# Kernel tuning notes

Measured on AMD Instinct MI355X. Metric: run time of the kernel, lower is better.

The kernel has to match this reference:

```python
import jax, jax.numpy as jnp
import numpy as np

N, E = 100000, 1600000
D_IN, D_HID, D_OUT = 128, 128, 64


def setup_inputs() -> dict:
    key = jax.random.key(0)
    ks = jax.random.split(key, 12)
    x = jax.random.normal(ks[0], (N, D_IN), dtype=jnp.float32)
    edge_index = jax.random.randint(ks[1], (2, E), 0, N, dtype=jnp.int32)

    def glorot(k, fan_in, fan_out):
        lim = np.sqrt(6.0 / (fan_in + fan_out)).astype(np.float32)
        return jax.random.uniform(k, (fan_in, fan_out), jnp.float32, -lim, lim)

    return {
        "x": x,
        "edge_index": edge_index,
        "W_l0": glorot(ks[2], D_IN, D_HID), "W_r0": glorot(ks[3], D_IN, D_HID), "b0": jnp.zeros((D_HID,), jnp.float32),
        "W_l1": glorot(ks[4], D_HID, D_HID), "W_r1": glorot(ks[5], D_HID, D_HID), "b1": jnp.zeros((D_HID,), jnp.float32),
        "W_l2": glorot(ks[6], D_HID, D_OUT), "W_r2": glorot(ks[7], D_HID, D_OUT), "b2": jnp.zeros((D_OUT,), jnp.float32),
    }


def _sage_conv(x, src, dst, W_l, W_r, b):
    # mean aggregation of source features onto destination nodes
    msg = jnp.take(x, src, axis=0)                               # [E, d]
    agg = jax.ops.segment_sum(msg, dst, num_segments=N)          # [N, d]
    deg = jax.ops.segment_sum(jnp.ones_like(dst, x.dtype), dst, num_segments=N)
    agg = agg / jnp.maximum(deg, 1.0)[:, None]
    # out = lin_l(aggr) + lin_r(x); lin_l has bias (PyG SAGEConv convention)
    return agg @ W_l + x @ W_r + b


def reference(x, edge_index, W_l0, W_r0, b0, W_l1, W_r1, b1, W_l2, W_r2, b2):
    src, dst = edge_index[0], edge_index[1]
    h = jax.nn.relu(_sage_conv(x, src, dst, W_l0, W_r0, b0))
    h = jax.nn.relu(_sage_conv(h, src, dst, W_l1, W_r1, b1))
    # dropout is identity in eval mode
    return _sage_conv(h, src, dst, W_l2, W_r2, b2)
```

## Files before the change

### kernel.cpp

```cpp
#include <hip/hip_runtime.h>
#include <hip/hip_bf16.h>
#include <stdint.h>

#define D 128
#define BSH 8
#define BKN 256
#define TILE 4096
#define CAPB 5376

typedef __attribute__((ext_vector_type(8))) short short8;
typedef __attribute__((ext_vector_type(4))) float f32x4;

typedef __attribute__((address_space(1))) const void gvoid;
typedef __attribute__((address_space(3))) void lvoid;

__device__ inline float bf16lo(uint32_t u){ return __uint_as_float(u << 16); }
__device__ inline float bf16hi(uint32_t u){ return __uint_as_float(u & 0xffff0000u); }
__device__ inline unsigned short f2bf(float f){
    union { __hip_bfloat16 h; unsigned short u; } cvt;
    cvt.h = __float2bfloat16(f);
    return cvt.u;
}

#define ACC8(q) \
    acc[0] += bf16lo(q.x); acc[1] += bf16hi(q.x); \
    acc[2] += bf16lo(q.y); acc[3] += bf16hi(q.y); \
    acc[4] += bf16lo(q.z); acc[5] += bf16hi(q.z); \
    acc[6] += bf16lo(q.w); acc[7] += bf16hi(q.w);

__global__ __launch_bounds__(256) void prep_and_bin(
    const int* __restrict__ src, const int* __restrict__ dst,
    int* __restrict__ bfill, uint32_t* __restrict__ binbuf, int E, int nbk, int nBin,
    const float* __restrict__ Wl0, const float* __restrict__ Wr0,
    const float* __restrict__ Wl1, const float* __restrict__ Wr1,
    const float* __restrict__ Wl2, const float* __restrict__ Wr2,
    unsigned short* __restrict__ WT0, unsigned short* __restrict__ WT1,
    unsigned short* __restrict__ WT2)
{
    __shared__ int hist[400];
    __shared__ int cur[400];
    int t = threadIdx.x;
    if ((int)blockIdx.x < nBin){
        int tile0 = blockIdx.x * TILE;
        int cnt = min(TILE, E - tile0);
        for (int i = t; i < nbk; i += 256) hist[i] = 0;
        __syncthreads();
        for (int i = t; i < cnt; i += 256)
            atomicAdd(&hist[dst[tile0 + i] >> BSH], 1);
        __syncthreads();
        for (int i = t; i < nbk; i += 256){
            int h = hist[i];
            int base = h ? atomicAdd(&bfill[i], h) : 0;
            cur[i] = i * CAPB + base;
        }
        __syncthreads();
        for (int i = t; i < cnt; i += 256){
            int d = dst[tile0 + i];
            int b = d >> BSH;
            int p = atomicAdd(&cur[b], 1);
            binbuf[p] = (uint32_t)src[tile0 + i] | ((uint32_t)(d & (BKN - 1)) << 17);
        }
    } else {
        int idx = ((int)blockIdx.x - nBin) * 256 + t;
        if (idx < 32768){
            int k = idx & 127, j = idx >> 7;
            WT0[j * 128 + k] = f2bf(j < 128 ? Wl0[k * 128 + j] : Wr0[k * 128 + (j - 128)]);
        } else if (idx < 65536){
            int i = idx - 32768; int k = i & 127, j = i >> 7;
            WT1[j * 128 + k] = f2bf(j < 128 ? Wl1[k * 128 + j] : Wr1[k * 128 + (j - 128)]);
        } else if (idx < 81920){
            int i = idx - 65536; int k = i & 127, j = i >> 7;
            WT2[j * 128 + k] = f2bf(j < 64 ? Wl2[k * 64 + j] : Wr2[k * 64 + (j - 64)]);
        }
    }
}

__global__ __launch_bounds__(256, 3) void gemm0_fill(
    const float* __restrict__ xf, const unsigned short* __restrict__ WT,
    const float* __restrict__ bias, unsigned short* __restrict__ ylz, int n,
    const uint32_t* __restrict__ binbuf, const int* __restrict__ bcnt,
    int* __restrict__ roff, int* __restrict__ rend, int* __restrict__ csr,
    int nbk, int gG)
{
    __shared__ __align__(16) char smem[128 * 256];
    int tid = threadIdx.x;

    if ((int)blockIdx.x < nbk){
        int* hist  = (int*)smem;
        int* hist2 = hist + 256;
        int* hb    = hist2 + 256;
        int* sc    = hb + 256;
        int b = blockIdx.x, t = tid;
        int e0 = b * CAPB;
        int e1 = e0 + bcnt[b];
        int v0 = b << BSH;
        int nv = min(BKN, n - v0);

        hist[t] = 0; hist2[t] = 0;
        __syncthreads();
        for (int e = e0 + t; e < e1; e += 256)
            atomicAdd(&hist[binbuf[e] >> 17], 1);
        __syncthreads();
        int own = hist[t];
        sc[t] = own;
        __syncthreads();
        for (int o = 1; o < 256; o <<= 1){
            int x = (t >= o) ? sc[t - o] : 0;
            __syncthreads();
            sc[t] += x;
            __syncthreads();
        }
        int ex = sc[t] - own;
        hb[t] = ex;
        if (t < nv){
            roff[v0 + t] = e0 + ex;
            rend[v0 + t] = e0 + ex + own;
        }
        __syncthreads();
        for (int e = e0 + t; e < e1; e += 256){
            uint32_t p = binbuf[e];
            int local = p >> 17;
            int pos = e0 + hb[local] + atomicAdd(&hist2[local], 1);
            csr[pos] = (int)(p & 0x1FFFFu);
        }
        return;
    }

    int bid = (int)blockIdx.x - nbk;
    int bx = bid % gG, by = bid / gG;
    char* As = smem;
    int lane = tid & 63, wave = tid >> 6;
    int rbase = bx * 128;
    int lrow = lane & 15, lk = (lane >> 4) * 8;
    int colbase = by * 128 + wave * 32;

    short8 bfr[4][2];
    #pragma unroll
    for (int kk = 0; kk < 4; kk++)
        #pragma unroll
        for (int cf = 0; cf < 2; cf++)
            bfr[kk][cf] = *reinterpret_cast<const short8*>(
                WT + (size_t)(colbase + cf * 16 + lrow) * 128 + kk * 32 + lk);

    {
        int cb = (tid & 15) * 16;
        #pragma unroll
        for (int i = 0; i < 8; i++){
            int row = i * 16 + (tid >> 4);
            int grow = min(rbase + row, n - 1);
            const float* p = xf + (size_t)grow * 128 + (cb >> 1);
            float4 f0 = *reinterpret_cast<const float4*>(p);
            float4 f1 = *reinterpret_cast<const float4*>(p + 4);
            uint4 q;
            q.x = (uint32_t)f2bf(f0.x) | ((uint32_t)f2bf(f0.y) << 16);
            q.y = (uint32_t)f2bf(f0.z) | ((uint32_t)f2bf(f0.w) << 16);
            q.z = (uint32_t)f2bf(f1.x) | ((uint32_t)f2bf(f1.y) << 16);
            q.w = (uint32_t)f2bf(f1.z) | ((uint32_t)f2bf(f1.w) << 16);
            *reinterpret_cast<uint4*>(As + row * 256 + (cb ^ ((row & 7) << 4))) = q;
        }
    }
    __syncthreads();

    f32x4 acc[8][2];
    #pragma unroll
    for (int fr = 0; fr < 8; fr++)
        #pragma unroll
        for (int cf = 0; cf < 2; cf++)
            acc[fr][cf] = (f32x4){0.f, 0.f, 0.f, 0.f};

    #pragma unroll
    for (int kk = 0; kk < 4; kk++){
        int cb = kk * 64 + (lane >> 4) * 16;
        #pragma unroll
        for (int fr = 0; fr < 8; fr++){
            int row = fr * 16 + lrow;
            short8 a = *reinterpret_cast<const short8*>(As + row * 256 + (cb ^ ((row & 7) << 4)));
            #pragma unroll
            for (int cf = 0; cf < 2; cf++)
                acc[fr][cf] = __builtin_amdgcn_mfma_f32_16x16x32_bf16(bfr[kk][cf], a, acc[fr][cf], 0, 0, 0);
        }
    }

    float4 bv[2];
    #pragma unroll
    for (int cf = 0; cf < 2; cf++){
        int cg = colbase + cf * 16 + (lane >> 4) * 4;
        bv[cf] = (cg >= 128) ? *reinterpret_cast<const float4*>(bias + (cg - 128))
                             : (float4){0.f, 0.f, 0.f, 0.f};
    }

    #pragma unroll
    for (int fr = 0; fr < 8; fr++){
        int row = rbase + fr * 16 + lrow;
        if (row < n){
            #pragma unroll
            for (int cf = 0; cf < 2; cf++){
                int cg = colbase + cf * 16 + (lane >> 4) * 4;
                uint2 o;
                o.x = (uint32_t)f2bf(acc[fr][cf][0] + bv[cf].x) |
                      ((uint32_t)f2bf(acc[fr][cf][1] + bv[cf].y) << 16);
                o.y = (uint32_t)f2bf(acc[fr][cf][2] + bv[cf].z) |
                      ((uint32_t)f2bf(acc[fr][cf][3] + bv[cf].w) << 16);
                *reinterpret_cast<uint2*>(ylz + (size_t)row * 256 + cg) = o;
            }
        }
    }
}

template<int NC>
__global__ __launch_bounds__(256, 3) void dense_gemm(
    const unsigned short* __restrict__ xb,
    const unsigned short* __restrict__ WT, const float* __restrict__ bias,
    unsigned short* __restrict__ ylz, int n)
{
    constexpr int DOUT = NC / 2;
    __shared__ __align__(16) char As[128 * 256];
    int tid = threadIdx.x, lane = tid & 63, wave = tid >> 6;
    int rbase = blockIdx.x * 128;
    int lrow = lane & 15, lk = (lane >> 4) * 8;
    int colbase = blockIdx.y * 128 + wave * 32;

    short8 bfr[4][2];
    #pragma unroll
    for (int kk = 0; kk < 4; kk++)
        #pragma unroll
        for (int cf = 0; cf < 2; cf++)
            bfr[kk][cf] = *reinterpret_cast<const short8*>(
                WT + (size_t)(colbase + cf * 16 + lrow) * 128 + kk * 32 + lk);

    {
        int cb = (lane & 15) * 16;
        #pragma unroll
        for (int i = 0; i < 8; i++){
            int row = i * 16 + (tid >> 4);
            int grow = min(rbase + row, n - 1);
            const unsigned short* gsrc = xb + (size_t)grow * 128 + ((cb ^ ((row & 7) << 4)) >> 1);
            __builtin_amdgcn_global_load_lds(
                (gvoid*)gsrc,
                (lvoid*)(As + (i * 16 + wave * 4) * 256),
                16, 0, 0);
        }
    }
    __syncthreads();

    f32x4 acc[8][2];
    #pragma unroll
    for (int fr = 0; fr < 8; fr++)
        #pragma unroll
        for (int cf = 0; cf < 2; cf++)
            acc[fr][cf] = (f32x4){0.f, 0.f, 0.f, 0.f};

    #pragma unroll
    for (int kk = 0; kk < 4; kk++){
        int cb = kk * 64 + (lane >> 4) * 16;
        #pragma unroll
        for (int fr = 0; fr < 8; fr++){
            int row = fr * 16 + lrow;
            short8 a = *reinterpret_cast<const short8*>(As + row * 256 + (cb ^ ((row & 7) << 4)));
            #pragma unroll
            for (int cf = 0; cf < 2; cf++)
                acc[fr][cf] = __builtin_amdgcn_mfma_f32_16x16x32_bf16(bfr[kk][cf], a, acc[fr][cf], 0, 0, 0);
        }
    }

    float4 bv[2];
    #pragma unroll
    for (int cf = 0; cf < 2; cf++){
        int cg = colbase + cf * 16 + (lane >> 4) * 4;
        bv[cf] = (cg >= DOUT) ? *reinterpret_cast<const float4*>(bias + (cg - DOUT))
                              : (float4){0.f, 0.f, 0.f, 0.f};
    }

    #pragma unroll
    for (int fr = 0; fr < 8; fr++){
        int row = rbase + fr * 16 + lrow;
        if (row < n){
            #pragma unroll
            for (int cf = 0; cf < 2; cf++){
                int cg = colbase + cf * 16 + (lane >> 4) * 4;
                uint2 o;
                o.x = (uint32_t)f2bf(acc[fr][cf][0] + bv[cf].x) |
                      ((uint32_t)f2bf(acc[fr][cf][1] + bv[cf].y) << 16);
                o.y = (uint32_t)f2bf(acc[fr][cf][2] + bv[cf].z) |
                      ((uint32_t)f2bf(acc[fr][cf][3] + bv[cf].w) << 16);
                *reinterpret_cast<uint2*>(ylz + (size_t)row * NC + cg) = o;
            }
        }
    }
}

__global__ __launch_bounds__(256, 4) void agg_relu(
    const unsigned short* __restrict__ ylz, const int* __restrict__ roff,
    const int* __restrict__ rend,
    const int* __restrict__ csr, unsigned short* __restrict__ hout, int n)
{
    int grp = threadIdx.x >> 4, li = threadIdx.x & 15;
    int v = blockIdx.x * 16 + grp;
    if (v >= n) return;
    int s0 = roff[v], s1 = rend[v];
    const unsigned short* base = ylz + li * 8;
    float acc[8] = {0.f,0.f,0.f,0.f,0.f,0.f,0.f,0.f};
    int e = s0;
    for (; e + 8 <= s1; e += 8){
        int i0=csr[e],i1=csr[e+1],i2=csr[e+2],i3=csr[e+3];
        int i4=csr[e+4],i5=csr[e+5],i6=csr[e+6],i7=csr[e+7];
        uint4 q0 = *reinterpret_cast<const uint4*>(base + (size_t)i0 * 256);
        uint4 q1 = *reinterpret_cast<const uint4*>(base + (size_t)i1 * 256);
        uint4 q2 = *reinterpret_cast<const uint4*>(base + (size_t)i2 * 256);
        uint4 q3 = *reinterpret_cast<const uint4*>(base + (size_t)i3 * 256);
        uint4 q4 = *reinterpret_cast<const uint4*>(base + (size_t)i4 * 256);
        uint4 q5 = *reinterpret_cast<const uint4*>(base + (size_t)i5 * 256);
        uint4 q6 = *reinterpret_cast<const uint4*>(base + (size_t)i6 * 256);
        uint4 q7 = *reinterpret_cast<const uint4*>(base + (size_t)i7 * 256);
        ACC8(q0) ACC8(q1) ACC8(q2) ACC8(q3) ACC8(q4) ACC8(q5) ACC8(q6) ACC8(q7)
    }
    if (e < s1){
        int last = s1 - 1;
        int i0=csr[e];
        int i1=csr[min(e+1,last)],i2=csr[min(e+2,last)],i3=csr[min(e+3,last)];
        int i4=csr[min(e+4,last)],i5=csr[min(e+5,last)],i6=csr[min(e+6,last)],i7=csr[min(e+7,last)];
        uint4 z4 = make_uint4(0,0,0,0);
        uint4 q0 = *reinterpret_cast<const uint4*>(base + (size_t)i0 * 256);
        uint4 q1 = *reinterpret_cast<const uint4*>(base + (size_t)i1 * 256);
        uint4 q2 = *reinterpret_cast<const uint4*>(base + (size_t)i2 * 256);
        uint4 q3 = *reinterpret_cast<const uint4*>(base + (size_t)i3 * 256);
        uint4 q4 = *reinterpret_cast<const uint4*>(base + (size_t)i4 * 256);
        uint4 q5 = *reinterpret_cast<const uint4*>(base + (size_t)i5 * 256);
        uint4 q6 = *reinterpret_cast<const uint4*>(base + (size_t)i6 * 256);
        uint4 q7 = *reinterpret_cast<const uint4*>(base + (size_t)i7 * 256);
        if (e+1 > last) q1 = z4;
        if (e+2 > last) q2 = z4;
        if (e+3 > last) q3 = z4;
        if (e+4 > last) q4 = z4;
        if (e+5 > last) q5 = z4;
        if (e+6 > last) q6 = z4;
        if (e+7 > last) q7 = z4;
        ACC8(q0) ACC8(q1) ACC8(q2) ACC8(q3) ACC8(q4) ACC8(q5) ACC8(q6) ACC8(q7)
    }
    int d = s1 - s0;
    float inv = (d > 0) ? 1.0f / (float)d : 0.0f;
    uint4 zq = *reinterpret_cast<const uint4*>(ylz + (size_t)v * 256 + 128 + li * 8);
    float z0=bf16lo(zq.x), z1=bf16hi(zq.x), z2=bf16lo(zq.y), z3=bf16hi(zq.y);
    float z4_=bf16lo(zq.z), z5=bf16hi(zq.z), z6=bf16lo(zq.w), z7=bf16hi(zq.w);
    uint4 o;
    o.x = (uint32_t)f2bf(fmaxf(acc[0]*inv+z0,0.f)) | ((uint32_t)f2bf(fmaxf(acc[1]*inv+z1,0.f)) << 16);
    o.y = (uint32_t)f2bf(fmaxf(acc[2]*inv+z2,0.f)) | ((uint32_t)f2bf(fmaxf(acc[3]*inv+z3,0.f)) << 16);
    o.z = (uint32_t)f2bf(fmaxf(acc[4]*inv+z4_,0.f)) | ((uint32_t)f2bf(fmaxf(acc[5]*inv+z5,0.f)) << 16);
    o.w = (uint32_t)f2bf(fmaxf(acc[6]*inv+z6,0.f)) | ((uint32_t)f2bf(fmaxf(acc[7]*inv+z7,0.f)) << 16);
    *reinterpret_cast<uint4*>(hout + (size_t)v * 128 + li * 8) = o;
}

__global__ __launch_bounds__(256, 4) void agg_out64(
    const unsigned short* __restrict__ ylz, const int* __restrict__ roff,
    const int* __restrict__ rend,
    const int* __restrict__ csr, float* __restrict__ out, int n)
{
    int grp = threadIdx.x >> 3, li = threadIdx.x & 7;
    int v = blockIdx.x * 32 + grp;
    if (v >= n) return;
    int s0 = roff[v], s1 = rend[v];
    const unsigned short* base = ylz + li * 8;
    float acc[8] = {0.f,0.f,0.f,0.f,0.f,0.f,0.f,0.f};
    int e = s0;
    for (; e + 8 <= s1; e += 8){
        int i0=csr[e],i1=csr[e+1],i2=csr[e+2],i3=csr[e+3];
        int i4=csr[e+4],i5=csr[e+5],i6=csr[e+6],i7=csr[e+7];
        uint4 q0 = *reinterpret_cast<const uint4*>(base + (size_t)i0 * 128);
        uint4 q1 = *reinterpret_cast<const uint4*>(base + (size_t)i1 * 128);
        uint4 q2 = *reinterpret_cast<const uint4*>(base + (size_t)i2 * 128);
        uint4 q3 = *reinterpret_cast<const uint4*>(base + (size_t)i3 * 128);
        uint4 q4 = *reinterpret_cast<const uint4*>(base + (size_t)i4 * 128);
        uint4 q5 = *reinterpret_cast<const uint4*>(base + (size_t)i5 * 128);
        uint4 q6 = *reinterpret_cast<const uint4*>(base + (size_t)i6 * 128);
        uint4 q7 = *reinterpret_cast<const uint4*>(base + (size_t)i7 * 128);
        ACC8(q0) ACC8(q1) ACC8(q2) ACC8(q3) ACC8(q4) ACC8(q5) ACC8(q6) ACC8(q7)
    }
    if (e < s1){
        int last = s1 - 1;
        int i0=csr[e];
        int i1=csr[min(e+1,last)],i2=csr[min(e+2,last)],i3=csr[min(e+3,last)];
        int i4=csr[min(e+4,last)],i5=csr[min(e+5,last)],i6=csr[min(e+6,last)],i7=csr[min(e+7,last)];
        uint4 z4 = make_uint4(0,0,0,0);
        uint4 q0 = *reinterpret_cast<const uint4*>(base + (size_t)i0 * 128);
        uint4 q1 = *reinterpret_cast<const uint4*>(base + (size_t)i1 * 128);
        uint4 q2 = *reinterpret_cast<const uint4*>(base + (size_t)i2 * 128);
        uint4 q3 = *reinterpret_cast<const uint4*>(base + (size_t)i3 * 128);
        uint4 q4 = *reinterpret_cast<const uint4*>(base + (size_t)i4 * 128);
        uint4 q5 = *reinterpret_cast<const uint4*>(base + (size_t)i5 * 128);
        uint4 q6 = *reinterpret_cast<const uint4*>(base + (size_t)i6 * 128);
        uint4 q7 = *reinterpret_cast<const uint4*>(base + (size_t)i7 * 128);
        if (e+1 > last) q1 = z4;
        if (e+2 > last) q2 = z4;
        if (e+3 > last) q3 = z4;
        if (e+4 > last) q4 = z4;
        if (e+5 > last) q5 = z4;
        if (e+6 > last) q6 = z4;
        if (e+7 > last) q7 = z4;
        ACC8(q0) ACC8(q1) ACC8(q2) ACC8(q3) ACC8(q4) ACC8(q5) ACC8(q6) ACC8(q7)
    }
    int d = s1 - s0;
    float inv = (d > 0) ? 1.0f / (float)d : 0.0f;
    uint4 zq = *reinterpret_cast<const uint4*>(ylz + (size_t)v * 128 + 64 + li * 8);
    float4 o0, o1;
    o0.x = acc[0]*inv + bf16lo(zq.x);
    o0.y = acc[1]*inv + bf16hi(zq.x);
    o0.z = acc[2]*inv + bf16lo(zq.y);
    o0.w = acc[3]*inv + bf16hi(zq.y);
    o1.x = acc[4]*inv + bf16lo(zq.z);
    o1.y = acc[5]*inv + bf16hi(zq.z);
    o1.z = acc[6]*inv + bf16lo(zq.w);
    o1.w = acc[7]*inv + bf16hi(zq.w);
    *reinterpret_cast<float4*>(out + (size_t)v * 64 + li * 8) = o0;
    *reinterpret_cast<float4*>(out + (size_t)v * 64 + li * 8 + 4) = o1;
}

extern "C" void kernel_launch(void* const* d_in, const int* in_sizes, int n_in,
                              void* d_out, int out_size, void* d_ws, size_t ws_size,
                              hipStream_t stream)
{
    const float* x   = (const float*)d_in[0];
    const int*   ei  = (const int*)d_in[1];
    const float* Wl0 = (const float*)d_in[2];
    const float* Wr0 = (const float*)d_in[3];
    const float* b0  = (const float*)d_in[4];
    const float* Wl1 = (const float*)d_in[5];
    const float* Wr1 = (const float*)d_in[6];
    const float* b1  = (const float*)d_in[7];
    const float* Wl2 = (const float*)d_in[8];
    const float* Wr2 = (const float*)d_in[9];
    const float* b2  = (const float*)d_in[10];

    int N = in_sizes[0] / D;
    int E = in_sizes[1] / 2;
    const int* src = ei;
    const int* dst = ei + E;
    int NBK = (N + BKN - 1) >> BSH;

    char* ws = (char*)d_ws;
    size_t off = 0;
    auto alloc = [&](size_t bytes) -> void* {
        void* p = ws + off;
        off = (off + bytes + 255) & ~(size_t)255;
        return p;
    };
    int*      bfill  = (int*)alloc((size_t)NBK * 4);
    int*      roff   = (int*)alloc((size_t)N * 4);
    int*      rend   = (int*)alloc((size_t)N * 4);
    int*      csr    = (int*)alloc((size_t)NBK * CAPB * 4);
    unsigned short* ylz = (unsigned short*)alloc((size_t)N * 256 * 2);
    unsigned short* h0  = (unsigned short*)alloc((size_t)N * D * 2);
    unsigned short* h1  = (unsigned short*)alloc((size_t)N * D * 2);
    unsigned short* WT0 = (unsigned short*)alloc((size_t)256 * 128 * 2);
    unsigned short* WT1 = (unsigned short*)alloc((size_t)256 * 128 * 2);
    unsigned short* WT2 = (unsigned short*)alloc((size_t)128 * 128 * 2);
    uint32_t* binbuf = (uint32_t*)alloc((size_t)NBK * CAPB * 4);

    hipMemsetAsync(bfill, 0, (size_t)NBK * 4, stream);

    int nBin = (E + TILE - 1) / TILE;
    int gG = (N + 127) / 128;
    int gA = (N + 15) / 16;
    int gA2 = (N + 31) / 32;

    prep_and_bin<<<nBin + 320, 256, 0, stream>>>(
        src, dst, bfill, binbuf, E, NBK, nBin,
        Wl0, Wr0, Wl1, Wr1, Wl2, Wr2, WT0, WT1, WT2);

    gemm0_fill<<<NBK + gG * 2, 256, 0, stream>>>(
        x, WT0, b0, ylz, N, binbuf, bfill, roff, rend, csr, NBK, gG);

    agg_relu<<<gA, 256, 0, stream>>>(ylz, roff, rend, csr, h0, N);
    dense_gemm<256><<<dim3(gG, 2), 256, 0, stream>>>(h0, WT1, b1, ylz, N);
    agg_relu<<<gA, 256, 0, stream>>>(ylz, roff, rend, csr, h1, N);
    dense_gemm<128><<<dim3(gG, 1), 256, 0, stream>>>(h1, WT2, b2, ylz, N);
    agg_out64<<<gA2, 256, 0, stream>>>(ylz, roff, rend, csr, (float*)d_out, N);
}
```

Baseline: 262.9 us.

## Store aggregated features in column-sliced layout so gathers hit compact per-slice arrays

The GEMM outputs that get gathered are now split into 8 feature slices of 16 (or 8) bf16 columns each, stored slice-major. Each aggregation block handles one slice for many nodes, so the working set of a gather pass is a small array that may stay in L2/MALL rather than striding across full rows. The root (z) half is written to a separate contiguous buffer. Buffers are aliased (binbuf onto h1sl, layer-2 outputs onto h0sl) to reduce the workspace footprint. In exchange, each edge index is now read 8 times, once per slice, and the GEMM input loads use a strided sliced addressing.

```diff
diff --git a/kernel.cpp b/kernel.cpp
--- a/kernel.cpp
+++ b/kernel.cpp
@@ -77,7 +77,8 @@
 
 __global__ __launch_bounds__(256, 3) void gemm0_fill(
     const float* __restrict__ xf, const unsigned short* __restrict__ WT,
-    const float* __restrict__ bias, unsigned short* __restrict__ ylz, int n,
+    const float* __restrict__ bias, unsigned short* __restrict__ ysl,
+    unsigned short* __restrict__ z, int n,
     const uint32_t* __restrict__ binbuf, const int* __restrict__ bcnt,
     int* __restrict__ roff, int* __restrict__ rend, int* __restrict__ csr,
     int nbk, int gG)
@@ -133,6 +134,7 @@
     int rbase = bx * 128;
     int lrow = lane & 15, lk = (lane >> 4) * 8;
     int colbase = by * 128 + wave * 32;
+    size_t n16 = (size_t)n * 16;
 
     short8 bfr[4][2];
     #pragma unroll
@@ -201,7 +203,10 @@
                       ((uint32_t)f2bf(acc[fr][cf][1] + bv[cf].y) << 16);
                 o.y = (uint32_t)f2bf(acc[fr][cf][2] + bv[cf].z) |
                       ((uint32_t)f2bf(acc[fr][cf][3] + bv[cf].w) << 16);
-                *reinterpret_cast<uint2*>(ylz + (size_t)row * 256 + cg) = o;
+                if (cg < 128)
+                    *reinterpret_cast<uint2*>(ysl + (size_t)(cg >> 4) * n16 + (size_t)row * 16 + (cg & 15)) = o;
+                else
+                    *reinterpret_cast<uint2*>(z + (size_t)row * 128 + (cg - 128)) = o;
             }
         }
     }
@@ -211,14 +216,17 @@
 __global__ __launch_bounds__(256, 3) void dense_gemm(
     const unsigned short* __restrict__ xb,
     const unsigned short* __restrict__ WT, const float* __restrict__ bias,
-    unsigned short* __restrict__ ylz, int n)
+    unsigned short* __restrict__ ysl, unsigned short* __restrict__ z, int n)
 {
     constexpr int DOUT = NC / 2;
+    constexpr int SL = DOUT / 8;
     __shared__ __align__(16) char As[128 * 256];
     int tid = threadIdx.x, lane = tid & 63, wave = tid >> 6;
     int rbase = blockIdx.x * 128;
     int lrow = lane & 15, lk = (lane >> 4) * 8;
     int colbase = blockIdx.y * 128 + wave * 32;
+    size_t n16 = (size_t)n * 16;
+    size_t nSL = (size_t)n * SL;
 
     short8 bfr[4][2];
     #pragma unroll
@@ -234,7 +242,9 @@
         for (int i = 0; i < 8; i++){
             int row = i * 16 + (tid >> 4);
             int grow = min(rbase + row, n - 1);
-            const unsigned short* gsrc = xb + (size_t)grow * 128 + ((cb ^ ((row & 7) << 4)) >> 1);
+            int cbx = cb ^ ((row & 7) << 4);
+            const unsigned short* gsrc = xb + (size_t)(cbx >> 5) * n16
+                                            + (size_t)grow * 16 + ((cbx & 31) >> 1);
             __builtin_amdgcn_global_load_lds(
                 (gvoid*)gsrc,
                 (lvoid*)(As + (i * 16 + wave * 4) * 256),
@@ -283,35 +293,39 @@
                       ((uint32_t)f2bf(acc[fr][cf][1] + bv[cf].y) << 16);
                 o.y = (uint32_t)f2bf(acc[fr][cf][2] + bv[cf].z) |
                       ((uint32_t)f2bf(acc[fr][cf][3] + bv[cf].w) << 16);
-                *reinterpret_cast<uint2*>(ylz + (size_t)row * NC + cg) = o;
+                if (cg < DOUT)
+                    *reinterpret_cast<uint2*>(ysl + (size_t)(cg / SL) * nSL + (size_t)row * SL + (cg % SL)) = o;
+                else
+                    *reinterpret_cast<uint2*>(z + (size_t)row * DOUT + (cg - DOUT)) = o;
             }
         }
     }
 }
 
-__global__ __launch_bounds__(256, 4) void agg_relu(
-    const unsigned short* __restrict__ ylz, const int* __restrict__ roff,
-    const int* __restrict__ rend,
-    const int* __restrict__ csr, unsigned short* __restrict__ hout, int n)
-{
-    int grp = threadIdx.x >> 4, li = threadIdx.x & 15;
-    int v = blockIdx.x * 16 + grp;
+__global__ __launch_bounds__(256, 4) void agg_relu_sl(
+    const unsigned short* __restrict__ ysl, const unsigned short* __restrict__ z,
+    const int* __restrict__ roff, const int* __restrict__ rend,
+    const int* __restrict__ csr, unsigned short* __restrict__ hsl, int n)
+{
+    int s = blockIdx.x & 7;
+    int v = (blockIdx.x >> 3) * 128 + (threadIdx.x >> 1);
+    int li2 = threadIdx.x & 1;
     if (v >= n) return;
     int s0 = roff[v], s1 = rend[v];
-    const unsigned short* base = ylz + li * 8;
+    const unsigned short* base = ysl + (size_t)s * ((size_t)n * 16) + li2 * 8;
     float acc[8] = {0.f,0.f,0.f,0.f,0.f,0.f,0.f,0.f};
     int e = s0;
     for (; e + 8 <= s1; e += 8){
         int i0=csr[e],i1=csr[e+1],i2=csr[e+2],i3=csr[e+3];
         int i4=csr[e+4],i5=csr[e+5],i6=csr[e+6],i7=csr[e+7];
-        uint4 q0 = *reinterpret_cast<const uint4*>(base + (size_t)i0 * 256);
-        uint4 q1 = *reinterpret_cast<const uint4*>(base + (size_t)i1 * 256);
-        uint4 q2 = *reinterpret_cast<const uint4*>(base + (size_t)i2 * 256);
-        uint4 q3 = *reinterpret_cast<const uint4*>(base + (size_t)i3 * 256);
-        uint4 q4 = *reinterpret_cast<const uint4*>(base + (size_t)i4 * 256);
-        uint4 q5 = *reinterpret_cast<const uint4*>(base + (size_t)i5 * 256);
-        uint4 q6 = *reinterpret_cast<const uint4*>(base + (size_t)i6 * 256);
-        uint4 q7 = *reinterpret_cast<const uint4*>(base + (size_t)i7 * 256);
+        uint4 q0 = *reinterpret_cast<const uint4*>(base + (size_t)i0 * 16);
+        uint4 q1 = *reinterpret_cast<const uint4*>(base + (size_t)i1 * 16);
+        uint4 q2 = *reinterpret_cast<const uint4*>(base + (size_t)i2 * 16);
+        uint4 q3 = *reinterpret_cast<const uint4*>(base + (size_t)i3 * 16);
+        uint4 q4 = *reinterpret_cast<const uint4*>(base + (size_t)i4 * 16);
+        uint4 q5 = *reinterpret_cast<const uint4*>(base + (size_t)i5 * 16);
+        uint4 q6 = *reinterpret_cast<const uint4*>(base + (size_t)i6 * 16);
+        uint4 q7 = *reinterpret_cast<const uint4*>(base + (size_t)i7 * 16);
         ACC8(q0) ACC8(q1) ACC8(q2) ACC8(q3) ACC8(q4) ACC8(q5) ACC8(q6) ACC8(q7)
     }
     if (e < s1){
@@ -320,14 +334,14 @@
         int i1=csr[min(e+1,last)],i2=csr[min(e+2,last)],i3=csr[min(e+3,last)];
         int i4=csr[min(e+4,last)],i5=csr[min(e+5,last)],i6=csr[min(e+6,last)],i7=csr[min(e+7,last)];
         uint4 z4 = make_uint4(0,0,0,0);
-        uint4 q0 = *reinterpret_cast<const uint4*>(base + (size_t)i0 * 256);
-        uint4 q1 = *reinterpret_cast<const uint4*>(base + (size_t)i1 * 256);
-        uint4 q2 = *reinterpret_cast<const uint4*>(base + (size_t)i2 * 256);
-        uint4 q3 = *reinterpret_cast<const uint4*>(base + (size_t)i3 * 256);
-        uint4 q4 = *reinterpret_cast<const uint4*>(base + (size_t)i4 * 256);
-        uint4 q5 = *reinterpret_cast<const uint4*>(base + (size_t)i5 * 256);
-        uint4 q6 = *reinterpret_cast<const uint4*>(base + (size_t)i6 * 256);
-        uint4 q7 = *reinterpret_cast<const uint4*>(base + (size_t)i7 * 256);
+        uint4 q0 = *reinterpret_cast<const uint4*>(base + (size_t)i0 * 16);
+        uint4 q1 = *reinterpret_cast<const uint4*>(base + (size_t)i1 * 16);
+        uint4 q2 = *reinterpret_cast<const uint4*>(base + (size_t)i2 * 16);
+        uint4 q3 = *reinterpret_cast<const uint4*>(base + (size_t)i3 * 16);
+        uint4 q4 = *reinterpret_cast<const uint4*>(base + (size_t)i4 * 16);
+        uint4 q5 = *reinterpret_cast<const uint4*>(base + (size_t)i5 * 16);
+        uint4 q6 = *reinterpret_cast<const uint4*>(base + (size_t)i6 * 16);
+        uint4 q7 = *reinterpret_cast<const uint4*>(base + (size_t)i7 * 16);
         if (e+1 > last) q1 = z4;
         if (e+2 > last) q2 = z4;
         if (e+3 > last) q3 = z4;
@@ -339,7 +353,7 @@
     }
     int d = s1 - s0;
     float inv = (d > 0) ? 1.0f / (float)d : 0.0f;
-    uint4 zq = *reinterpret_cast<const uint4*>(ylz + (size_t)v * 256 + 128 + li * 8);
+    uint4 zq = *reinterpret_cast<const uint4*>(z + (size_t)v * 128 + s * 16 + li2 * 8);
     float z0=bf16lo(zq.x), z1=bf16hi(zq.x), z2=bf16lo(zq.y), z3=bf16hi(zq.y);
     float z4_=bf16lo(zq.z), z5=bf16hi(zq.z), z6=bf16lo(zq.w), z7=bf16hi(zq.w);
     uint4 o;
@@ -347,32 +361,32 @@
     o.y = (uint32_t)f2bf(fmaxf(acc[2]*inv+z2,0.f)) | ((uint32_t)f2bf(fmaxf(acc[3]*inv+z3,0.f)) << 16);
     o.z = (uint32_t)f2bf(fmaxf(acc[4]*inv+z4_,0.f)) | ((uint32_t)f2bf(fmaxf(acc[5]*inv+z5,0.f)) << 16);
     o.w = (uint32_t)f2bf(fmaxf(acc[6]*inv+z6,0.f)) | ((uint32_t)f2bf(fmaxf(acc[7]*inv+z7,0.f)) << 16);
-    *reinterpret_cast<uint4*>(hout + (size_t)v * 128 + li * 8) = o;
-}
-
-__global__ __launch_bounds__(256, 4) void agg_out64(
-    const unsigned short* __restrict__ ylz, const int* __restrict__ roff,
-    const int* __restrict__ rend,
+    *reinterpret_cast<uint4*>(hsl + (size_t)s * ((size_t)n * 16) + (size_t)v * 16 + li2 * 8) = o;
+}
+
+__global__ __launch_bounds__(256, 4) void agg_out64_sl(
+    const unsigned short* __restrict__ ysl2, const unsigned short* __restrict__ z2,
+    const int* __restrict__ roff, const int* __restrict__ rend,
     const int* __restrict__ csr, float* __restrict__ out, int n)
 {
-    int grp = threadIdx.x >> 3, li = threadIdx.x & 7;
-    int v = blockIdx.x * 32 + grp;
+    int s = blockIdx.x & 7;
+    int v = (blockIdx.x >> 3) * 256 + threadIdx.x;
     if (v >= n) return;
     int s0 = roff[v], s1 = rend[v];
-    const unsigned short* base = ylz + li * 8;
+    const unsigned short* base = ysl2 + (size_t)s * ((size_t)n * 8);
     float acc[8] = {0.f,0.f,0.f,0.f,0.f,0.f,0.f,0.f};
     int e = s0;
     for (; e + 8 <= s1; e += 8){
         int i0=csr[e],i1=csr[e+1],i2=csr[e+2],i3=csr[e+3];
         int i4=csr[e+4],i5=csr[e+5],i6=csr[e+6],i7=csr[e+7];
-        uint4 q0 = *reinterpret_cast<const uint4*>(base + (size_t)i0 * 128);
-        uint4 q1 = *reinterpret_cast<const uint4*>(base + (size_t)i1 * 128);
-        uint4 q2 = *reinterpret_cast<const uint4*>(base + (size_t)i2 * 128);
-        uint4 q3 = *reinterpret_cast<const uint4*>(base + (size_t)i3 * 128);
-        uint4 q4 = *reinterpret_cast<const uint4*>(base + (size_t)i4 * 128);
-        uint4 q5 = *reinterpret_cast<const uint4*>(base + (size_t)i5 * 128);
-        uint4 q6 = *reinterpret_cast<const uint4*>(base + (size_t)i6 * 128);
-        uint4 q7 = *reinterpret_cast<const uint4*>(base + (size_t)i7 * 128);
+        uint4 q0 = *reinterpret_cast<const uint4*>(base + (size_t)i0 * 8);
+        uint4 q1 = *reinterpret_cast<const uint4*>(base + (size_t)i1 * 8);
+        uint4 q2 = *reinterpret_cast<const uint4*>(base + (size_t)i2 * 8);
+        uint4 q3 = *reinterpret_cast<const uint4*>(base + (size_t)i3 * 8);
+        uint4 q4 = *reinterpret_cast<const uint4*>(base + (size_t)i4 * 8);
+        uint4 q5 = *reinterpret_cast<const uint4*>(base + (size_t)i5 * 8);
+        uint4 q6 = *reinterpret_cast<const uint4*>(base + (size_t)i6 * 8);
+        uint4 q7 = *reinterpret_cast<const uint4*>(base + (size_t)i7 * 8);
         ACC8(q0) ACC8(q1) ACC8(q2) ACC8(q3) ACC8(q4) ACC8(q5) ACC8(q6) ACC8(q7)
     }
     if (e < s1){
@@ -381,14 +395,14 @@
         int i1=csr[min(e+1,last)],i2=csr[min(e+2,last)],i3=csr[min(e+3,last)];
         int i4=csr[min(e+4,last)],i5=csr[min(e+5,last)],i6=csr[min(e+6,last)],i7=csr[min(e+7,last)];
         uint4 z4 = make_uint4(0,0,0,0);
-        uint4 q0 = *reinterpret_cast<const uint4*>(base + (size_t)i0 * 128);
-        uint4 q1 = *reinterpret_cast<const uint4*>(base + (size_t)i1 * 128);
-        uint4 q2 = *reinterpret_cast<const uint4*>(base + (size_t)i2 * 128);
-        uint4 q3 = *reinterpret_cast<const uint4*>(base + (size_t)i3 * 128);
-        uint4 q4 = *reinterpret_cast<const uint4*>(base + (size_t)i4 * 128);
-        uint4 q5 = *reinterpret_cast<const uint4*>(base + (size_t)i5 * 128);
-        uint4 q6 = *reinterpret_cast<const uint4*>(base + (size_t)i6 * 128);
-        uint4 q7 = *reinterpret_cast<const uint4*>(base + (size_t)i7 * 128);
+        uint4 q0 = *reinterpret_cast<const uint4*>(base + (size_t)i0 * 8);
+        uint4 q1 = *reinterpret_cast<const uint4*>(base + (size_t)i1 * 8);
+        uint4 q2 = *reinterpret_cast<const uint4*>(base + (size_t)i2 * 8);
+        uint4 q3 = *reinterpret_cast<const uint4*>(base + (size_t)i3 * 8);
+        uint4 q4 = *reinterpret_cast<const uint4*>(base + (size_t)i4 * 8);
+        uint4 q5 = *reinterpret_cast<const uint4*>(base + (size_t)i5 * 8);
+        uint4 q6 = *reinterpret_cast<const uint4*>(base + (size_t)i6 * 8);
+        uint4 q7 = *reinterpret_cast<const uint4*>(base + (size_t)i7 * 8);
         if (e+1 > last) q1 = z4;
         if (e+2 > last) q2 = z4;
         if (e+3 > last) q3 = z4;
@@ -400,7 +414,7 @@
     }
     int d = s1 - s0;
     float inv = (d > 0) ? 1.0f / (float)d : 0.0f;
-    uint4 zq = *reinterpret_cast<const uint4*>(ylz + (size_t)v * 128 + 64 + li * 8);
+    uint4 zq = *reinterpret_cast<const uint4*>(z2 + (size_t)v * 64 + s * 8);
     float4 o0, o1;
     o0.x = acc[0]*inv + bf16lo(zq.x);
     o0.y = acc[1]*inv + bf16hi(zq.x);
@@ -410,8 +424,8 @@
     o1.y = acc[5]*inv + bf16hi(zq.z);
     o1.z = acc[6]*inv + bf16lo(zq.w);
     o1.w = acc[7]*inv + bf16hi(zq.w);
-    *reinterpret_cast<float4*>(out + (size_t)v * 64 + li * 8) = o0;
-    *reinterpret_cast<float4*>(out + (size_t)v * 64 + li * 8 + 4) = o1;
+    *reinterpret_cast<float4*>(out + (size_t)v * 64 + s * 8) = o0;
+    *reinterpret_cast<float4*>(out + (size_t)v * 64 + s * 8 + 4) = o1;
 }
 
 extern "C" void kernel_launch(void* const* d_in, const int* in_sizes, int n_in,
@@ -447,31 +461,34 @@
     int*      roff   = (int*)alloc((size_t)N * 4);
     int*      rend   = (int*)alloc((size_t)N * 4);
     int*      csr    = (int*)alloc((size_t)NBK * CAPB * 4);
-    unsigned short* ylz = (unsigned short*)alloc((size_t)N * 256 * 2);
-    unsigned short* h0  = (unsigned short*)alloc((size_t)N * D * 2);
-    unsigned short* h1  = (unsigned short*)alloc((size_t)N * D * 2);
+    unsigned short* ysl  = (unsigned short*)alloc((size_t)N * 128 * 2);
+    unsigned short* z    = (unsigned short*)alloc((size_t)N * 128 * 2);
+    unsigned short* h0sl = (unsigned short*)alloc((size_t)N * 128 * 2);
+    unsigned short* h1sl = (unsigned short*)alloc((size_t)N * 128 * 2);
     unsigned short* WT0 = (unsigned short*)alloc((size_t)256 * 128 * 2);
     unsigned short* WT1 = (unsigned short*)alloc((size_t)256 * 128 * 2);
     unsigned short* WT2 = (unsigned short*)alloc((size_t)128 * 128 * 2);
-    uint32_t* binbuf = (uint32_t*)alloc((size_t)NBK * CAPB * 4);
+    uint32_t* binbuf = (uint32_t*)h1sl;
+    unsigned short* ysl2 = h0sl;
+    unsigned short* z2   = h0sl + (size_t)N * 64;
 
     hipMemsetAsync(bfill, 0, (size_t)NBK * 4, stream);
 
     int nBin = (E + TILE - 1) / TILE;
     int gG = (N + 127) / 128;
-    int gA = (N + 15) / 16;
-    int gA2 = (N + 31) / 32;
+    int gAs  = 8 * ((N + 127) / 128);
+    int gAs2 = 8 * ((N + 255) / 256);
 
     prep_and_bin<<<nBin + 320, 256, 0, stream>>>(
         src, dst, bfill, binbuf, E, NBK, nBin,
         Wl0, Wr0, Wl1, Wr1, Wl2, Wr2, WT0, WT1, WT2);
 
     gemm0_fill<<<NBK + gG * 2, 256, 0, stream>>>(
-        x, WT0, b0, ylz, N, binbuf, bfill, roff, rend, csr, NBK, gG);
-
-    agg_relu<<<gA, 256, 0, stream>>>(ylz, roff, rend, csr, h0, N);
-    dense_gemm<256><<<dim3(gG, 2), 256, 0, stream>>>(h0, WT1, b1, ylz, N);
-    agg_relu<<<gA, 256, 0, stream>>>(ylz, roff, rend, csr, h1, N);
-    dense_gemm<128><<<dim3(gG, 1), 256, 0, stream>>>(h1, WT2, b2, ylz, N);
-    agg_out64<<<gA2, 256, 0, stream>>>(ylz, roff, rend, csr, (float*)d_out, N);
-}
+        x, WT0, b0, ysl, z, N, binbuf, bfill, roff, rend, csr, NBK, gG);
+
+    agg_relu_sl<<<gAs, 256, 0, stream>>>(ysl, z, roff, rend, csr, h0sl, N);
+    dense_gemm<256><<<dim3(gG, 2), 256, 0, stream>>>(h0sl, WT1, b1, ysl, z, N);
+    agg_relu_sl<<<gAs, 256, 0, stream>>>(ysl, z, roff, rend, csr, h1sl, N);
+    dense_gemm<128><<<dim3(gG, 1), 256, 0, stream>>>(h1sl, WT2, b2, ysl2, z2, N);
+    agg_out64_sl<<<gAs2, 256, 0, stream>>>(ysl2, z2, roff, rend, csr, (float*)d_out, N);
+}
```

Result: slower. 377.0 us (+43.4%).
